# Kernel optimization log

Hardware: AMD Instinct MI355X
Metric: run time of the kernel (lower is better)

The kernel has to match this reference:

```python
import jax, jax.numpy as jnp
import numpy as np

B = 64          # number of scenes/graphs
OBJS = 2048     # objects per scene
N = B * OBJS    # total objects
D = 256         # representation_dim
K = 2           # num_channels


def setup_inputs() -> dict:
    key = jax.random.key(0)
    k1, k2, k3 = jax.random.split(key, 3)
    x_aggregation = jax.random.normal(k1, (N, D), dtype=jnp.float32)
    num_objs = jnp.full((B,), OBJS, dtype=jnp.int32)
    # glorot for att_shared [1, D]: fan_in + fan_out = 1 + D
    std_shared = float(np.sqrt(6.0 / (1 + D)))
    att_shared = jax.random.uniform(k2, (1, D), dtype=jnp.float32,
                                    minval=-std_shared, maxval=std_shared)
    # glorot for att_scale [K, 1]
    std_scale = float(np.sqrt(6.0 / (K + 1)))
    att_scale = jax.random.uniform(k3, (K, 1), dtype=jnp.float32,
                                   minval=-std_scale, maxval=std_scale)
    channel_bias = jnp.zeros((K, D), dtype=jnp.float32)
    return {"x_aggregation": x_aggregation, "num_objs": num_objs,
            "att_shared": att_shared, "att_scale": att_scale,
            "channel_bias": channel_bias}


def reference(x_aggregation, num_objs, att_shared, att_scale, channel_bias):
    batch_idx = jnp.repeat(jnp.arange(B), num_objs, total_repeat_length=N)  # [N]
    # scatter_mean: per-scene context features [B, D]
    seg_sum = jax.ops.segment_sum(x_aggregation, batch_idx, num_segments=B)
    counts = jnp.maximum(num_objs, 1).astype(x_aggregation.dtype)
    ctx = seg_sum / counts[:, None]
    attn_in = jax.nn.leaky_relu(x_aggregation + ctx[batch_idx], negative_slope=0.2)  # [N, D]
    # per-channel logits: ((attn_in + bias[k]) . att_shared) * scale[k]
    base = attn_in @ att_shared[0]                 # [N]
    bias_term = channel_bias @ att_shared[0]       # [K]
    logits = (base[:, None] + bias_term[None, :]) * att_scale[:, 0][None, :]  # [N, K]
    # per-channel segment softmax over objects within each scene
    m = jax.ops.segment_max(logits, batch_idx, num_segments=B)   # [B, K]
    z = jnp.exp(logits - m[batch_idx])
    s = jax.ops.segment_sum(z, batch_idx, num_segments=B)        # [B, K]
    attn_weights = z / s[batch_idx]                              # [N, K]
    # attention-weighted pooling per channel -> [B, D, K]
    weighted = x_aggregation[:, :, None] * attn_weights[:, None, :]  # [N, D, K]
    scene_features = jax.ops.segment_sum(weighted, batch_idx, num_segments=B)
    return scene_features, attn_weights
```

## Files before the change

### kernel.cpp

```cpp
#include <hip/hip_runtime.h>

#define B    64
#define OBJS 2048
#define NTOT (B * OBJS)
#define D    256
#define K    2
#define S1   16
#define CH   (OBJS / S1)
#define RPW  (CH / 4)

#define WS_UP  0
#define WS_P1  0
#define WS_CTX 524288
#define WS_BT  540672
#define WS_ZP  540736
#define WS_Z   548928
#define WS_E   549056

static __device__ __forceinline__ float lrelu02(float v) {
    return v > 0.0f ? v : 0.2f * v;
}

__global__ __launch_bounds__(256) void k1_partial(const float* __restrict__ x,
                                                  float* __restrict__ ws) {
    __shared__ float red[4 * D];
    int blk = blockIdx.x;
    int b = blk >> 4, c = blk & 15;
    int w = threadIdx.x >> 6, l = threadIdx.x & 63;
    int row0 = b * OBJS + c * CH + w * RPW;

    float4 acc = make_float4(0.f, 0.f, 0.f, 0.f);
    const float* px = x + (size_t)row0 * D + 4 * l;
#pragma unroll 4
    for (int j = 0; j < RPW; ++j) {
        float4 v = *(const float4*)(px + (size_t)j * D);
        acc.x += v.x; acc.y += v.y; acc.z += v.z; acc.w += v.w;
    }
    *(float4*)(red + w * D + 4 * l) = acc;
    __syncthreads();
    int t = threadIdx.x;
    if (t < 64) {
        float4 a = ((const float4*)(red        ))[t];
        float4 e = ((const float4*)(red +     D))[t];
        float4 f = ((const float4*)(red + 2 * D))[t];
        float4 g = ((const float4*)(red + 3 * D))[t];
        float4 s = make_float4(a.x + e.x + f.x + g.x, a.y + e.y + f.y + g.y,
                               a.z + e.z + f.z + g.z, a.w + e.w + f.w + g.w);
        *(float4*)(ws + WS_P1 + blk * D + 4 * t) = s;
    }
}

__global__ __launch_bounds__(256) void k1b_reduce(const float* __restrict__ att_shared,
                                                  const float* __restrict__ channel_bias,
                                                  const int* __restrict__ num_objs,
                                                  float* __restrict__ ws) {
    int b = blockIdx.x, t = threadIdx.x;
    int cnt = num_objs[b]; if (cnt < 1) cnt = 1;
    float inv = 1.0f / (float)cnt;
    float s = 0.f;
#pragma unroll
    for (int c = 0; c < S1; ++c) s += ws[WS_P1 + (b * S1 + c) * D + t];
    ws[WS_CTX + b * D + t] = s * inv;

    if (b == 0 && t < 64) {
        float4 a = ((const float4*)att_shared)[t];
#pragma unroll
        for (int k = 0; k < K; ++k) {
            float4 cb = ((const float4*)(channel_bias + k * D))[t];
            float v = a.x * cb.x + a.y * cb.y + a.z * cb.z + a.w * cb.w;
#pragma unroll
            for (int m = 32; m > 0; m >>= 1) v += __shfl_xor(v, m);
            if (t == 0) ws[WS_BT + k] = v;
        }
    }
}

__global__ __launch_bounds__(256) void k2_main(const float* __restrict__ x,
                                               const float* __restrict__ att_scale,
                                               const float* __restrict__ att_shared,
                                               float* __restrict__ ws) {
    __shared__ float ured[4 * D * K];
    int blk = blockIdx.x;
    int b = blk >> 4, c = blk & 15;
    int w = threadIdx.x >> 6, l = threadIdx.x & 63;
    int row0 = b * OBJS + c * CH + w * RPW;

    float4 a4 = ((const float4*)att_shared)[l];
    float4 ctx4 = *(const float4*)(ws + WS_CTX + b * D + 4 * l);
    float bt0 = ws[WS_BT + 0], bt1 = ws[WS_BT + 1];
    float s0 = att_scale[0],   s1 = att_scale[1];

    float4 acc0 = make_float4(0.f, 0.f, 0.f, 0.f);
    float4 acc1 = make_float4(0.f, 0.f, 0.f, 0.f);
    float z0 = 0.f, z1 = 0.f;
    float my_e0 = 0.f, my_e1 = 0.f;
    int sel = l & 31;
    const float* px = x + (size_t)row0 * D + 4 * l;

#pragma unroll 2
    for (int j = 0; j < RPW; ++j) {
        float4 v = *(const float4*)(px + (size_t)j * D);
        float p = lrelu02(v.x + ctx4.x) * a4.x
                + lrelu02(v.y + ctx4.y) * a4.y
                + lrelu02(v.z + ctx4.z) * a4.z
                + lrelu02(v.w + ctx4.w) * a4.w;
#pragma unroll
        for (int m = 32; m > 0; m >>= 1) p += __shfl_xor(p, m);
        float e0 = __expf((p + bt0) * s0);
        float e1 = __expf((p + bt1) * s1);
        z0 += e0; z1 += e1;
        acc0.x += v.x * e0; acc0.y += v.y * e0; acc0.z += v.z * e0; acc0.w += v.w * e0;
        acc1.x += v.x * e1; acc1.y += v.y * e1; acc1.z += v.z * e1; acc1.w += v.w * e1;
        if (j == sel) { my_e0 = e0; my_e1 = e1; }
    }

    if (l < 32) ((float2*)(ws + WS_E))[row0 + l] = make_float2(my_e0, my_e1);
    if (l == 0) {
        ws[WS_ZP + blk * 8 + w * 2 + 0] = z0;
        ws[WS_ZP + blk * 8 + w * 2 + 1] = z1;
    }
    int base = w * (D * K) + l * 8;
    ured[base + 0] = acc0.x; ured[base + 1] = acc1.x;
    ured[base + 2] = acc0.y; ured[base + 3] = acc1.y;
    ured[base + 4] = acc0.z; ured[base + 5] = acc1.z;
    ured[base + 6] = acc0.w; ured[base + 7] = acc1.w;
    __syncthreads();
    int t = threadIdx.x;
    if (t < 128) {
        float4 a = ((const float4*)(ured       ))[t];
        float4 e = ((const float4*)(ured +  512))[t];
        float4 f = ((const float4*)(ured + 1024))[t];
        float4 g = ((const float4*)(ured + 1536))[t];
        float4 s = make_float4(a.x + e.x + f.x + g.x, a.y + e.y + f.y + g.y,
                               a.z + e.z + f.z + g.z, a.w + e.w + f.w + g.w);
        *(float4*)(ws + WS_UP + blk * (D * K) + 4 * t) = s;
    }
}

__global__ void kz_reduce(float* __restrict__ ws) {
    int t = threadIdx.x;
    int b = t >> 1, k = t & 1;
    float s = 0.f;
    for (int c = 0; c < S1; ++c)
#pragma unroll
        for (int w = 0; w < 4; ++w)
            s += ws[WS_ZP + (b * S1 + c) * 8 + w * 2 + k];
    ws[WS_Z + t] = s;
}

__global__ __launch_bounds__(256) void k3_final(const float* __restrict__ ws,
                                                float* __restrict__ out) {
    int i = blockIdx.x * 256 + threadIdx.x;
    const int FEAT = B * D * K;
    if (i < FEAT) {
        int b = i >> 9;
        int j = i & 511;
        int k = i & 1;
        float s = 0.f;
#pragma unroll
        for (int c = 0; c < S1; ++c) s += ws[WS_UP + (b * S1 + c) * 512 + j];
        out[i] = s / ws[WS_Z + b * K + k];
    } else {
        int r = i - FEAT;
        if (r < NTOT) {
            int b = r >> 11;
            float2 e = ((const float2*)(ws + WS_E))[r];
            float z0 = ws[WS_Z + b * K + 0];
            float z1 = ws[WS_Z + b * K + 1];
            ((float2*)(out + FEAT))[r] = make_float2(e.x / z0, e.y / z1);
        }
    }
}

extern "C" void kernel_launch(void* const* d_in, const int* in_sizes, int n_in,
                              void* d_out, int out_size, void* d_ws, size_t ws_size,
                              hipStream_t stream) {
    const float* x            = (const float*)d_in[0];
    const int*   num_objs     = (const int*)d_in[1];
    const float* att_shared   = (const float*)d_in[2];
    const float* att_scale    = (const float*)d_in[3];
    const float* channel_bias = (const float*)d_in[4];
    float* ws  = (float*)d_ws;
    float* out = (float*)d_out;

    k1_partial<<<B * S1, 256, 0, stream>>>(x, ws);
    k1b_reduce<<<B, 256, 0, stream>>>(att_shared, channel_bias, num_objs, ws);
    k2_main<<<B * S1, 256, 0, stream>>>(x, att_scale, att_shared, ws);
    kz_reduce<<<1, 128, 0, stream>>>(ws);
    const int total = B * D * K + NTOT;
    k3_final<<<(total + 255) / 256, 256, 0, stream>>>(ws, out);
}
```

Before: 227.3 us.

## Fuse context and z reductions into neighbouring kernels, cutting launches from five to three

The per-scene context mean and bias-term dot product are now computed in shared memory at the start of each main block instead of in a separate kernel. The z-sum reduction is folded into the final kernel, which now runs one block per scene. Workspace partials for P1 and UP no longer alias, and unroll factors rise in the two streaming loops. This removes two kernel launches and their serialization gaps, at the cost of each of the 1024 main blocks redundantly reading 16 partial context rows.

```diff
diff --git a/kernel.cpp b/kernel.cpp
--- a/kernel.cpp
+++ b/kernel.cpp
@@ -9,13 +9,10 @@
 #define CH   (OBJS / S1)
 #define RPW  (CH / 4)
 
-#define WS_UP  0
 #define WS_P1  0
-#define WS_CTX 524288
-#define WS_BT  540672
-#define WS_ZP  540736
-#define WS_Z   548928
-#define WS_E   549056
+#define WS_UP  (1024 * 256)
+#define WS_ZP  (WS_UP + 1024 * 512)
+#define WS_E   (WS_ZP + 1024 * 8)
 
 static __device__ __forceinline__ float lrelu02(float v) {
     return v > 0.0f ? v : 0.2f * v;
@@ -25,13 +22,12 @@
                                                   float* __restrict__ ws) {
     __shared__ float red[4 * D];
     int blk = blockIdx.x;
-    int b = blk >> 4, c = blk & 15;
     int w = threadIdx.x >> 6, l = threadIdx.x & 63;
-    int row0 = b * OBJS + c * CH + w * RPW;
+    int row0 = blk * CH + w * RPW;
 
     float4 acc = make_float4(0.f, 0.f, 0.f, 0.f);
     const float* px = x + (size_t)row0 * D + 4 * l;
-#pragma unroll 4
+#pragma unroll 8
     for (int j = 0; j < RPW; ++j) {
         float4 v = *(const float4*)(px + (size_t)j * D);
         acc.x += v.x; acc.y += v.y; acc.z += v.z; acc.w += v.w;
@@ -50,19 +46,30 @@
     }
 }
 
-__global__ __launch_bounds__(256) void k1b_reduce(const float* __restrict__ att_shared,
-                                                  const float* __restrict__ channel_bias,
-                                                  const int* __restrict__ num_objs,
-                                                  float* __restrict__ ws) {
-    int b = blockIdx.x, t = threadIdx.x;
-    int cnt = num_objs[b]; if (cnt < 1) cnt = 1;
-    float inv = 1.0f / (float)cnt;
-    float s = 0.f;
+__global__ __launch_bounds__(256) void k2_main(const float* __restrict__ x,
+                                               const int* __restrict__ num_objs,
+                                               const float* __restrict__ att_scale,
+                                               const float* __restrict__ att_shared,
+                                               const float* __restrict__ channel_bias,
+                                               float* __restrict__ ws) {
+    __shared__ float sctx[D];
+    __shared__ float sbt[2];
+    __shared__ float ured[4 * D * K];
+    int blk = blockIdx.x;
+    int b = blk >> 4;
+    int t = threadIdx.x;
+    int w = t >> 6, l = t & 63;
+    int row0 = blk * CH + w * RPW;
+
+    {
+        int cnt = num_objs[b]; if (cnt < 1) cnt = 1;
+        float inv = 1.0f / (float)cnt;
+        float s = 0.f;
 #pragma unroll
-    for (int c = 0; c < S1; ++c) s += ws[WS_P1 + (b * S1 + c) * D + t];
-    ws[WS_CTX + b * D + t] = s * inv;
-
-    if (b == 0 && t < 64) {
+        for (int c = 0; c < S1; ++c) s += ws[WS_P1 + (b * S1 + c) * D + t];
+        sctx[t] = s * inv;
+    }
+    if (t < 64) {
         float4 a = ((const float4*)att_shared)[t];
 #pragma unroll
         for (int k = 0; k < K; ++k) {
@@ -70,25 +77,15 @@
             float v = a.x * cb.x + a.y * cb.y + a.z * cb.z + a.w * cb.w;
 #pragma unroll
             for (int m = 32; m > 0; m >>= 1) v += __shfl_xor(v, m);
-            if (t == 0) ws[WS_BT + k] = v;
+            if (t == 0) sbt[k] = v;
         }
     }
-}
-
-__global__ __launch_bounds__(256) void k2_main(const float* __restrict__ x,
-                                               const float* __restrict__ att_scale,
-                                               const float* __restrict__ att_shared,
-                                               float* __restrict__ ws) {
-    __shared__ float ured[4 * D * K];
-    int blk = blockIdx.x;
-    int b = blk >> 4, c = blk & 15;
-    int w = threadIdx.x >> 6, l = threadIdx.x & 63;
-    int row0 = b * OBJS + c * CH + w * RPW;
+    __syncthreads();
 
     float4 a4 = ((const float4*)att_shared)[l];
-    float4 ctx4 = *(const float4*)(ws + WS_CTX + b * D + 4 * l);
-    float bt0 = ws[WS_BT + 0], bt1 = ws[WS_BT + 1];
-    float s0 = att_scale[0],   s1 = att_scale[1];
+    float4 ctx4 = *(const float4*)(sctx + 4 * l);
+    float bt0 = sbt[0], bt1 = sbt[1];
+    float s0 = att_scale[0], s1 = att_scale[1];
 
     float4 acc0 = make_float4(0.f, 0.f, 0.f, 0.f);
     float4 acc1 = make_float4(0.f, 0.f, 0.f, 0.f);
@@ -97,7 +94,7 @@
     int sel = l & 31;
     const float* px = x + (size_t)row0 * D + 4 * l;
 
-#pragma unroll 2
+#pragma unroll 4
     for (int j = 0; j < RPW; ++j) {
         float4 v = *(const float4*)(px + (size_t)j * D);
         float p = lrelu02(v.x + ctx4.x) * a4.x
@@ -125,7 +122,6 @@
     ured[base + 4] = acc0.z; ured[base + 5] = acc1.z;
     ured[base + 6] = acc0.w; ured[base + 7] = acc1.w;
     __syncthreads();
-    int t = threadIdx.x;
     if (t < 128) {
         float4 a = ((const float4*)(ured       ))[t];
         float4 e = ((const float4*)(ured +  512))[t];
@@ -137,38 +133,35 @@
     }
 }
 
-__global__ void kz_reduce(float* __restrict__ ws) {
-    int t = threadIdx.x;
-    int b = t >> 1, k = t & 1;
-    float s = 0.f;
-    for (int c = 0; c < S1; ++c)
-#pragma unroll
-        for (int w = 0; w < 4; ++w)
-            s += ws[WS_ZP + (b * S1 + c) * 8 + w * 2 + k];
-    ws[WS_Z + t] = s;
-}
-
 __global__ __launch_bounds__(256) void k3_final(const float* __restrict__ ws,
                                                 float* __restrict__ out) {
-    int i = blockIdx.x * 256 + threadIdx.x;
-    const int FEAT = B * D * K;
-    if (i < FEAT) {
-        int b = i >> 9;
-        int j = i & 511;
-        int k = i & 1;
+    __shared__ float zsh[2];
+    int b = blockIdx.x;
+    int t = threadIdx.x;
+    int w = t >> 6, l = t & 63;
+
+    if (w < 2) {
+        float v = ws[WS_ZP + (b * S1 + (l >> 2)) * 8 + (l & 3) * 2 + w];
+#pragma unroll
+        for (int m = 32; m > 0; m >>= 1) v += __shfl_xor(v, m);
+        if (l == 0) zsh[w] = v;
+    }
+    __syncthreads();
+    float z0 = zsh[0], z1 = zsh[1];
+
+#pragma unroll
+    for (int j = t; j < D * K; j += 256) {
         float s = 0.f;
 #pragma unroll
-        for (int c = 0; c < S1; ++c) s += ws[WS_UP + (b * S1 + c) * 512 + j];
-        out[i] = s / ws[WS_Z + b * K + k];
-    } else {
-        int r = i - FEAT;
-        if (r < NTOT) {
-            int b = r >> 11;
-            float2 e = ((const float2*)(ws + WS_E))[r];
-            float z0 = ws[WS_Z + b * K + 0];
-            float z1 = ws[WS_Z + b * K + 1];
-            ((float2*)(out + FEAT))[r] = make_float2(e.x / z0, e.y / z1);
-        }
+        for (int c = 0; c < S1; ++c) s += ws[WS_UP + (b * S1 + c) * (D * K) + j];
+        out[b * (D * K) + j] = s / ((j & 1) ? z1 : z0);
+    }
+    const float2* E = (const float2*)(ws + WS_E);
+    float2* W = (float2*)(out + B * D * K);
+#pragma unroll
+    for (int i = t; i < OBJS; i += 256) {
+        float2 e = E[b * OBJS + i];
+        W[b * OBJS + i] = make_float2(e.x / z0, e.y / z1);
     }
 }
 
@@ -184,9 +177,7 @@
     float* out = (float*)d_out;
 
     k1_partial<<<B * S1, 256, 0, stream>>>(x, ws);
-    k1b_reduce<<<B, 256, 0, stream>>>(att_shared, channel_bias, num_objs, ws);
-    k2_main<<<B * S1, 256, 0, stream>>>(x, att_scale, att_shared, ws);
-    kz_reduce<<<1, 128, 0, stream>>>(ws);
-    const int total = B * D * K + NTOT;
-    k3_final<<<(total + 255) / 256, 256, 0, stream>>>(ws, out);
+    k2_main<<<B * S1, 256, 0, stream>>>(x, num_objs, att_scale, att_shared,
+                                        channel_bias, ws);
+    k3_final<<<B, 256, 0, stream>>>(ws, out);
 }
```

Result: faster. 222.8 us (-2.0%).
